# Performance work log

Measured on AMD Instinct MI355X. Metric: run time of the kernel, lower is better.

## Reference

```python
import jax, jax.numpy as jnp
import numpy as np

E = 32      # num_embodiments
A = 64      # action_dim
H = 1024    # hidden_size
B = 64
T = 64


def setup_inputs() -> dict:
    key = jax.random.key(0)
    ks = jax.random.split(key, 9)
    return {
        "actions": jax.random.normal(ks[0], (B, T, A), dtype=jnp.float32),
        "W1_W": 0.02 * jax.random.normal(ks[1], (E, A, H), dtype=jnp.float32),
        "W1_b": jnp.zeros((E, H), dtype=jnp.float32),
        "W2_W": 0.02 * jax.random.normal(ks[2], (E, 2 * H, H), dtype=jnp.float32),
        "W2_b": jnp.zeros((E, H), dtype=jnp.float32),
        "W3_W": 0.02 * jax.random.normal(ks[3], (E, H, H), dtype=jnp.float32),
        "W3_b": jnp.zeros((E, H), dtype=jnp.float32),
        "timesteps": jax.random.randint(ks[4], (B,), 0, 1000, dtype=jnp.int32),
        "cat_ids": jax.random.randint(ks[5], (B,), 0, E, dtype=jnp.int32),
    }


def _cat_linear(x, W, b, cat_ids):
    # x: (B,T,in), W: (E,in,out), b: (E,out)
    Wg = W[cat_ids]               # (B,in,out) gathered per-batch weights
    bg = b[cat_ids]               # (B,out)
    return jnp.einsum('bti,bio->bto', x, Wg) + bg[:, None, :]


def _sinusoidal_pe(t, dim):
    # t: (B,T) float -> (B,T,dim)
    half = dim // 2
    exponent = -jnp.arange(half, dtype=jnp.float32) * (jnp.log(jnp.float32(10000.0)) / half)
    freqs = t[..., None] * jnp.exp(exponent)
    return jnp.concatenate([jnp.sin(freqs), jnp.cos(freqs)], axis=-1)


def reference(actions, W1_W, W1_b, W2_W, W2_b, W3_W, W3_b, timesteps, cat_ids):
    b, t, _ = actions.shape
    ts = jnp.broadcast_to(timesteps.astype(jnp.float32)[:, None], (b, t))  # (B,T)
    a_emb = _cat_linear(actions, W1_W, W1_b, cat_ids)                      # (B,T,H)
    tau_emb = _sinusoidal_pe(ts, H).astype(a_emb.dtype)                    # (B,T,H)
    x = jnp.concatenate([a_emb, tau_emb], axis=-1)                         # (B,T,2H)
    h = _cat_linear(x, W2_W, W2_b, cat_ids)
    x = h * jax.nn.sigmoid(h)                                              # swish
    return _cat_linear(x, W3_W, W3_b, cat_ids)                             # (B,T,H)
```

## Files before the change

kernel.cpp:

```cpp
#include <hip/hip_runtime.h>
#include <hip/hip_bf16.h>

#define NB 64
#define NT 64
#define NA 64
#define NH 1024
#define NE 32
#define K2DIM 2048

typedef unsigned short bf16_t;
typedef __attribute__((ext_vector_type(8))) short bf16x8;
typedef __attribute__((ext_vector_type(4))) short s16x4;
typedef __attribute__((ext_vector_type(4))) float f32x4;

__device__ __forceinline__ bf16_t f32_to_bf16(float f) {
    unsigned int u = __float_as_uint(f);
    u = (u + 0x7FFFu + ((u >> 16) & 1u)) >> 16;
    return (bf16_t)u;
}
__device__ __forceinline__ unsigned cvt2(float x, float y) {
    unsigned short a = __builtin_bit_cast(unsigned short, __float2bfloat16(x));
    unsigned short b = __builtin_bit_cast(unsigned short, __float2bfloat16(y));
    return (unsigned)a | ((unsigned)b << 16);
}

__global__ void make_groups(const int* __restrict__ cat_ids,
                            int* __restrict__ groups)
{
    __shared__ int keys[NB], order[NB], catv[NB];
    __shared__ int gcat[NB], gnb[NB], gb[NB][2];
    __shared__ int sng;

    const int tid = threadIdx.x;
    int c = cat_ids[tid];
    catv[tid] = c;
    keys[tid] = c * 64 + tid;
    __syncthreads();

    int mykey = keys[tid];
    int rank = 0;
    for (int j = 0; j < NB; ++j) rank += (keys[j] < mykey) ? 1 : 0;
    order[rank] = tid;
    __syncthreads();

    if (tid == 0) {
        int ng = 0, prev = -1, cnt = 2;
        for (int i = 0; i < NB; ++i) {
            int b  = order[i];
            int cb = catv[b];
            if (cb != prev || cnt == 2) {
                gcat[ng] = cb; gnb[ng] = 0; cnt = 0; prev = cb; ++ng;
            }
            gb[ng - 1][cnt] = b;
            ++cnt; gnb[ng - 1] = cnt;
        }
        sng = ng;
    }
    __syncthreads();

    int ng = sng;
    int base = tid * 8;
    if (tid < ng) {
        int nbv = gnb[tid];
        groups[base + 0] = gcat[tid];
        groups[base + 1] = nbv;
        groups[base + 2] = gb[tid][0];
        groups[base + 3] = (nbv > 1) ? gb[tid][1] : gb[tid][0];
        groups[base + 4] = 0; groups[base + 5] = 0;
        groups[base + 6] = 0; groups[base + 7] = 0;
    } else {
        #pragma unroll
        for (int s = 0; s < 8; ++s) groups[base + s] = 0;
    }
}

__global__ __launch_bounds__(256) void k1_embed(
    const float* __restrict__ actions, const float* __restrict__ W1,
    const float* __restrict__ b1, const int* __restrict__ timesteps,
    const int* __restrict__ cat_ids, bf16_t* __restrict__ x)
{
    __shared__ float act[NT][NA];
    __shared__ float pe[64];

    const int b   = blockIdx.x;
    const int c0  = blockIdx.y * 64;
    const int tid = threadIdx.x;
    const int cat = cat_ids[b];
    const float ts = (float)timesteps[b];

    const float* ab = actions + b * (NT * NA);
    #pragma unroll
    for (int p = 0; p < 16; ++p) {
        int idx = tid + p * 256;
        act[idx >> 6][idx & 63] = ab[idx];
    }
    if (tid < 64) {
        const float kfreq = logf(10000.0f) / 512.0f;
        int c = c0 + tid;
        float v;
        if (c < 512) v = sinf(ts * expf(-(float)c * kfreq));
        else         v = cosf(ts * expf(-(float)(c - 512) * kfreq));
        pe[tid] = v;
    }
    __syncthreads();

    const int cc = tid & 63;
    const int c  = c0 + cc;
    const int t0 = tid >> 6;

    float acc[16];
    const float bias = b1[cat * NH + c];
    #pragma unroll
    for (int i = 0; i < 16; ++i) acc[i] = bias;

    const float* Wp = W1 + (size_t)cat * (NA * NH) + c;
    #pragma unroll 8
    for (int k = 0; k < NA; ++k) {
        float w = Wp[(size_t)k * NH];
        #pragma unroll
        for (int i = 0; i < 16; ++i)
            acc[i] = fmaf(act[t0 + 4 * i][k], w, acc[i]);
    }

    bf16_t* xb = x + (size_t)b * (NT * K2DIM);
    const bf16_t pv = f32_to_bf16(pe[cc]);
    #pragma unroll
    for (int i = 0; i < 16; ++i) {
        int t = t0 + 4 * i;
        xb[(size_t)t * K2DIM + c]      = f32_to_bf16(acc[i]);
        xb[(size_t)t * K2DIM + NH + c] = pv;
    }
}

template<int KDIM, bool SWISH, typename OutT>
__global__ __launch_bounds__(512, 4) void gemm_g2(
    const bf16_t* __restrict__ xin, const float* __restrict__ W,
    const float* __restrict__ bias, const int* __restrict__ groups,
    OutT* __restrict__ out)
{
    __shared__ __align__(128) char lds[2][12288];

    const int* grp = groups + blockIdx.y * 8;
    const int nb = grp[1];
    if (nb == 0) return;
    const int cat = grp[0];
    const int ba = grp[2];
    const int bb = grp[3];

    const int n0   = blockIdx.x * 64;
    const int tid  = threadIdx.x;
    const int lane = tid & 63;
    const int wv   = tid >> 6;
    const int l15  = lane & 15;
    const int l4   = lane >> 4;
    const int slot = wv >> 2;
    const int nf   = wv & 3;

    constexpr int NCH = KDIM / 32;

    const int xs_s = tid >> 8;
    const int xid  = tid & 255;
    const int xt   = xid >> 2;
    const int xoct = xid & 3;
    const bf16_t* xg = xin + ((size_t)(xs_s ? bb : ba) * NT + xt) * KDIM + xoct * 8;
    const int xl = xs_s * 4096 + xoct * 1024 + xt * 16;

    const int wk  = tid >> 4;
    const int wq4 = tid & 15;
    const float* wg = W + (size_t)cat * KDIM * NH + (size_t)wk * NH + n0 + wq4 * 4;
    const int wl = 8192 + ((wk >> 2) * 4 + (wq4 >> 2)) * 128
                        + (wk & 3) * 32 + (wq4 & 3) * 8;

    f32x4 acc[4];
    {
        float bv = bias[(size_t)cat * NH + n0 + nf * 16 + l15];
        #pragma unroll
        for (int mf = 0; mf < 4; ++mf) acc[mf] = (f32x4){bv, bv, bv, bv};
    }

    const unsigned ldsbase = (unsigned)(unsigned long long)&lds[0][0];
    const unsigned trb = ldsbase + 8192u + (unsigned)(l4 * 1024 + nf * 128 + l15 * 8);
    const int aoff = slot * 4096 + l4 * 1024 + l15 * 16;

    uint4  xr;
    float4 wr;
    auto LOAD = [&](int kc) {
        xr = *(const uint4*)(xg + (size_t)kc * 32);
        wr = *(const float4*)(wg + (size_t)kc * 32 * NH);
    };
    auto WRITE = [&](int pw) {
        *(uint4*)(&lds[pw][0] + xl) = xr;
        uint2 pk;
        pk.x = cvt2(wr.x, wr.y);
        pk.y = cvt2(wr.z, wr.w);
        *(uint2*)(&lds[pw][0] + wl) = pk;
    };

    LOAD(0);
    WRITE(0);
    LOAD(1);

    for (int kc = 0; kc < NCH; ++kc) {
        const int p = kc & 1;
        __syncthreads();

        bf16x8 af0 = *(const bf16x8*)(&lds[p][0] + aoff);
        bf16x8 af1 = *(const bf16x8*)(&lds[p][0] + aoff + 256);
        bf16x8 af2 = *(const bf16x8*)(&lds[p][0] + aoff + 512);
        bf16x8 af3 = *(const bf16x8*)(&lds[p][0] + aoff + 768);
        unsigned a = trb + (unsigned)(p * 12288);
        s16x4 lo, hi;
        asm volatile("ds_read_b64_tr_b16 %0, %1" : "=v"(lo) : "v"(a));
        asm volatile("ds_read_b64_tr_b16 %0, %1 offset:512" : "=v"(hi) : "v"(a));
        bf16x8 bfr = __builtin_shufflevector(lo, hi, 0, 1, 2, 3, 4, 5, 6, 7);

        asm volatile("s_waitcnt lgkmcnt(0)" ::: "memory");
        __builtin_amdgcn_sched_barrier(0);
        acc[0] = __builtin_amdgcn_mfma_f32_16x16x32_bf16(af0, bfr, acc[0], 0, 0, 0);
        acc[1] = __builtin_amdgcn_mfma_f32_16x16x32_bf16(af1, bfr, acc[1], 0, 0, 0);
        acc[2] = __builtin_amdgcn_mfma_f32_16x16x32_bf16(af2, bfr, acc[2], 0, 0, 0);
        acc[3] = __builtin_amdgcn_mfma_f32_16x16x32_bf16(af3, bfr, acc[3], 0, 0, 0);

        if (kc + 1 < NCH) WRITE(p ^ 1);
        if (kc + 2 < NCH) LOAD(kc + 2);
    }

    if (slot < nb) {
        const int bout = slot ? bb : ba;
        const int col  = n0 + nf * 16 + l15;
        #pragma unroll
        for (int mf = 0; mf < 4; ++mf) {
            #pragma unroll
            for (int r = 0; r < 4; ++r) {
                int trow = mf * 16 + l4 * 4 + r;
                float h = acc[mf][r];
                if (SWISH) h = h / (1.0f + __expf(-h));
                if constexpr (sizeof(OutT) == 2) {
                    out[((size_t)bout * NT + trow) * NH + col] = (OutT)f32_to_bf16(h);
                } else {
                    out[((size_t)bout * NT + trow) * NH + col] = h;
                }
            }
        }
    }
}

extern "C" void kernel_launch(void* const* d_in, const int* in_sizes, int n_in,
                              void* d_out, int out_size, void* d_ws, size_t ws_size,
                              hipStream_t stream) {
    const float* actions   = (const float*)d_in[0];
    const float* W1        = (const float*)d_in[1];
    const float* b1        = (const float*)d_in[2];
    const float* W2        = (const float*)d_in[3];
    const float* b2        = (const float*)d_in[4];
    const float* W3        = (const float*)d_in[5];
    const float* b3        = (const float*)d_in[6];
    const int*   timesteps = (const int*)d_in[7];
    const int*   cat_ids   = (const int*)d_in[8];
    float* out = (float*)d_out;

    bf16_t* x = (bf16_t*)d_ws;
    bf16_t* y = x + (size_t)NB * NT * K2DIM;
    int* groups = (int*)(y + (size_t)NB * NT * NH);

    make_groups<<<1, 64, 0, stream>>>(cat_ids, groups);
    k1_embed<<<dim3(NB, NH / 64), 256, 0, stream>>>(actions, W1, b1, timesteps, cat_ids, x);
    gemm_g2<K2DIM, true,  bf16_t><<<dim3(16, 64), 512, 0, stream>>>(x, W2, b2, groups, y);
    gemm_g2<NH,    false, float ><<<dim3(16, 64), 512, 0, stream>>>(y, W3, b3, groups, out);
}
```

Baseline: 176.7 us.

## Narrow grouped GEMM N tile to 32, double K chunk, deepen weight prefetch

The grouped GEMM kernels now use 256-thread blocks that each cover 32 output columns instead of 64, which doubles the grid to 32x64 blocks. Each K step now processes 64 instead of 32, with two MFMA substeps per LDS buffer. Weights are prefetched two chunks ahead in registers, with the loop manually unrolled over ping-pong buffers. The aim is more blocks in flight and better latency hiding for the fp32 weight stream, at the cost of more LDS per block, more registers, and activation tiles being reloaded by twice as many blocks.

```diff
diff --git a/kernel.cpp b/kernel.cpp
--- a/kernel.cpp
+++ b/kernel.cpp
@@ -133,12 +133,12 @@
 }
 
 template<int KDIM, bool SWISH, typename OutT>
-__global__ __launch_bounds__(512, 4) void gemm_g2(
+__global__ __launch_bounds__(256, 3) void gemm_g2p(
     const bf16_t* __restrict__ xin, const float* __restrict__ W,
     const float* __restrict__ bias, const int* __restrict__ groups,
     OutT* __restrict__ out)
 {
-    __shared__ __align__(128) char lds[2][12288];
+    __shared__ __align__(128) char lds[2][20480];
 
     const int* grp = groups + blockIdx.y * 8;
     const int nb = grp[1];
@@ -147,29 +147,28 @@
     const int ba = grp[2];
     const int bb = grp[3];
 
-    const int n0   = blockIdx.x * 64;
+    const int n0   = blockIdx.x * 32;
     const int tid  = threadIdx.x;
     const int lane = tid & 63;
     const int wv   = tid >> 6;
     const int l15  = lane & 15;
     const int l4   = lane >> 4;
-    const int slot = wv >> 2;
-    const int nf   = wv & 3;
-
-    constexpr int NCH = KDIM / 32;
-
-    const int xs_s = tid >> 8;
-    const int xid  = tid & 255;
-    const int xt   = xid >> 2;
-    const int xoct = xid & 3;
-    const bf16_t* xg = xin + ((size_t)(xs_s ? bb : ba) * NT + xt) * KDIM + xoct * 8;
-    const int xl = xs_s * 4096 + xoct * 1024 + xt * 16;
-
-    const int wk  = tid >> 4;
-    const int wq4 = tid & 15;
-    const float* wg = W + (size_t)cat * KDIM * NH + (size_t)wk * NH + n0 + wq4 * 4;
-    const int wl = 8192 + ((wk >> 2) * 4 + (wq4 >> 2)) * 128
-                        + (wk & 3) * 32 + (wq4 & 3) * 8;
+    const int slot = wv >> 1;
+    const int nf   = wv & 1;
+
+    constexpr int NCH = KDIM / 64;
+
+    const int xs_s = tid >> 7;
+    const int xt   = (tid >> 1) & 63;
+    const int xoh  = tid & 1;
+    const bf16_t* xg = xin + ((size_t)(xs_s ? bb : ba) * NT + xt) * KDIM + xoh * 32;
+    const int xl = xs_s * 8192 + xoh * 4096 + xt * 16;
+
+    const int wk   = tid >> 2;
+    const int woct = tid & 3;
+    const float* wg = W + (size_t)cat * KDIM * NH + (size_t)wk * NH + n0 + woct * 8;
+    const int wl = 16384 + (wk >> 5) * 2048 + ((wk & 31) >> 2) * 256
+                 + (woct >> 1) * 128 + (wk & 3) * 32 + (woct & 1) * 16;
 
     f32x4 acc[4];
     {
@@ -179,50 +178,77 @@
     }
 
     const unsigned ldsbase = (unsigned)(unsigned long long)&lds[0][0];
-    const unsigned trb = ldsbase + 8192u + (unsigned)(l4 * 1024 + nf * 128 + l15 * 8);
-    const int aoff = slot * 4096 + l4 * 1024 + l15 * 16;
-
-    uint4  xr;
-    float4 wr;
-    auto LOAD = [&](int kc) {
-        xr = *(const uint4*)(xg + (size_t)kc * 32);
-        wr = *(const float4*)(wg + (size_t)kc * 32 * NH);
-    };
-    auto WRITE = [&](int pw) {
-        *(uint4*)(&lds[pw][0] + xl) = xr;
-        uint2 pk;
-        pk.x = cvt2(wr.x, wr.y);
-        pk.y = cvt2(wr.z, wr.w);
-        *(uint2*)(&lds[pw][0] + wl) = pk;
-    };
-
-    LOAD(0);
-    WRITE(0);
-    LOAD(1);
-
-    for (int kc = 0; kc < NCH; ++kc) {
-        const int p = kc & 1;
+    const unsigned trb0 = ldsbase + 16384u
+                        + (unsigned)(l4 * 512 + nf * 128 + l15 * 8);
+    const int aoff = slot * 8192 + l4 * 1024 + l15 * 16;
+
+    uint4  xr[4];
+    float4 wa[2], wb[2];
+
+    auto XLOAD = [&](int c) {
+        int i = c < NCH ? c : NCH - 1;
+        const bf16_t* s = xg + (size_t)i * 64;
+        #pragma unroll
+        for (int p_ = 0; p_ < 4; ++p_) xr[p_] = *(const uint4*)(s + p_ * 8);
+    };
+    auto XWRITE = [&](char* buf) {
+        #pragma unroll
+        for (int p_ = 0; p_ < 4; ++p_)
+            *(uint4*)(buf + xl + p_ * 1024) = xr[p_];
+    };
+    auto WLOAD = [&](float4* w, int c) {
+        int i = c < NCH ? c : NCH - 1;
+        const float* s = wg + (size_t)i * 64 * NH;
+        w[0] = *(const float4*)(s);
+        w[1] = *(const float4*)(s + 4);
+    };
+    auto WWRITE = [&](char* buf, const float4* w) {
+        uint4 pk;
+        pk.x = cvt2(w[0].x, w[0].y);
+        pk.y = cvt2(w[0].z, w[0].w);
+        pk.z = cvt2(w[1].x, w[1].y);
+        pk.w = cvt2(w[1].z, w[1].w);
+        *(uint4*)(buf + wl) = pk;
+    };
+    auto COMPUTE = [&](int p) {
+        char* buf = &lds[0][0] + p * 20480;
+        unsigned trp = trb0 + (unsigned)(p * 20480);
+        #pragma unroll
+        for (int ks = 0; ks < 2; ++ks) {
+            bf16x8 af[4];
+            #pragma unroll
+            for (int mf = 0; mf < 4; ++mf)
+                af[mf] = *(const bf16x8*)(buf + aoff + ks * 4096 + mf * 256);
+            unsigned a = trp + (unsigned)(ks * 2048);
+            s16x4 lo, hi;
+            asm volatile("ds_read_b64_tr_b16 %0, %1" : "=v"(lo) : "v"(a));
+            asm volatile("ds_read_b64_tr_b16 %0, %1 offset:256" : "=v"(hi) : "v"(a));
+            bf16x8 bfr = __builtin_shufflevector(lo, hi, 0, 1, 2, 3, 4, 5, 6, 7);
+            asm volatile("s_waitcnt lgkmcnt(0)" ::: "memory");
+            __builtin_amdgcn_sched_barrier(0);
+            #pragma unroll
+            for (int mf = 0; mf < 4; ++mf)
+                acc[mf] = __builtin_amdgcn_mfma_f32_16x16x32_bf16(
+                    af[mf], bfr, acc[mf], 0, 0, 0);
+        }
+    };
+
+    char* buf0 = &lds[0][0];
+    char* buf1 = &lds[0][0] + 20480;
+
+    WLOAD(wa, 0); WLOAD(wb, 1); XLOAD(0);
+    WWRITE(buf0, wa); XWRITE(buf0);
+    WLOAD(wa, 2); XLOAD(1);
+
+    for (int kc = 0; kc < NCH; kc += 2) {
         __syncthreads();
-
-        bf16x8 af0 = *(const bf16x8*)(&lds[p][0] + aoff);
-        bf16x8 af1 = *(const bf16x8*)(&lds[p][0] + aoff + 256);
-        bf16x8 af2 = *(const bf16x8*)(&lds[p][0] + aoff + 512);
-        bf16x8 af3 = *(const bf16x8*)(&lds[p][0] + aoff + 768);
-        unsigned a = trb + (unsigned)(p * 12288);
-        s16x4 lo, hi;
-        asm volatile("ds_read_b64_tr_b16 %0, %1" : "=v"(lo) : "v"(a));
-        asm volatile("ds_read_b64_tr_b16 %0, %1 offset:512" : "=v"(hi) : "v"(a));
-        bf16x8 bfr = __builtin_shufflevector(lo, hi, 0, 1, 2, 3, 4, 5, 6, 7);
-
-        asm volatile("s_waitcnt lgkmcnt(0)" ::: "memory");
-        __builtin_amdgcn_sched_barrier(0);
-        acc[0] = __builtin_amdgcn_mfma_f32_16x16x32_bf16(af0, bfr, acc[0], 0, 0, 0);
-        acc[1] = __builtin_amdgcn_mfma_f32_16x16x32_bf16(af1, bfr, acc[1], 0, 0, 0);
-        acc[2] = __builtin_amdgcn_mfma_f32_16x16x32_bf16(af2, bfr, acc[2], 0, 0, 0);
-        acc[3] = __builtin_amdgcn_mfma_f32_16x16x32_bf16(af3, bfr, acc[3], 0, 0, 0);
-
-        if (kc + 1 < NCH) WRITE(p ^ 1);
-        if (kc + 2 < NCH) LOAD(kc + 2);
+        COMPUTE(0);
+        WWRITE(buf1, wb); XWRITE(buf1);
+        WLOAD(wb, kc + 3); XLOAD(kc + 2);
+        __syncthreads();
+        COMPUTE(1);
+        WWRITE(buf0, wa); XWRITE(buf0);
+        WLOAD(wa, kc + 4); XLOAD(kc + 3);
     }
 
     if (slot < nb) {
@@ -265,6 +291,6 @@
 
     make_groups<<<1, 64, 0, stream>>>(cat_ids, groups);
     k1_embed<<<dim3(NB, NH / 64), 256, 0, stream>>>(actions, W1, b1, timesteps, cat_ids, x);
-    gemm_g2<K2DIM, true,  bf16_t><<<dim3(16, 64), 512, 0, stream>>>(x, W2, b2, groups, y);
-    gemm_g2<NH,    false, float ><<<dim3(16, 64), 512, 0, stream>>>(y, W3, b3, groups, out);
-}
+    gemm_g2p<K2DIM, true,  bf16_t><<<dim3(32, 64), 256, 0, stream>>>(x, W2, b2, groups, y);
+    gemm_g2p<NH,    false, float ><<<dim3(32, 64), 256, 0, stream>>>(y, W3, b3, groups, out);
+}
```

New measurement: 395.3 us. 2.24x slower.

## Group up to four batches per category and stream weights via LDS per wave

Applied to the files above, without the earlier changes.

Batches are now grouped up to four per embodiment instead of two, so each block reuses one weight tile across more batches and fewer redundant weight reads hit global memory. The GEMM is restructured: each of four waves owns one batch and computes a full 64x64 output tile. Activations are loaded straight from global memory into registers, and only the weights are staged in LDS, in 64-wide K chunks with a double-buffered register prefetch. The risks are higher register pressure from 16 accumulators and uncoalesced direct activation loads.

```diff
diff --git a/kernel.cpp b/kernel.cpp
--- a/kernel.cpp
+++ b/kernel.cpp
@@ -28,7 +28,7 @@
                             int* __restrict__ groups)
 {
     __shared__ int keys[NB], order[NB], catv[NB];
-    __shared__ int gcat[NB], gnb[NB], gb[NB][2];
+    __shared__ int gcat[NB], gnb[NB], gb[NB][4];
     __shared__ int sng;
 
     const int tid = threadIdx.x;
@@ -44,11 +44,11 @@
     __syncthreads();
 
     if (tid == 0) {
-        int ng = 0, prev = -1, cnt = 2;
+        int ng = 0, prev = -1, cnt = 4;
         for (int i = 0; i < NB; ++i) {
             int b  = order[i];
             int cb = catv[b];
-            if (cb != prev || cnt == 2) {
+            if (cb != prev || cnt == 4) {
                 gcat[ng] = cb; gnb[ng] = 0; cnt = 0; prev = cb; ++ng;
             }
             gb[ng - 1][cnt] = b;
@@ -64,9 +64,9 @@
         int nbv = gnb[tid];
         groups[base + 0] = gcat[tid];
         groups[base + 1] = nbv;
-        groups[base + 2] = gb[tid][0];
-        groups[base + 3] = (nbv > 1) ? gb[tid][1] : gb[tid][0];
-        groups[base + 4] = 0; groups[base + 5] = 0;
+        #pragma unroll
+        for (int s = 0; s < 4; ++s)
+            groups[base + 2 + s] = gb[tid][s < nbv ? s : 0];
         groups[base + 6] = 0; groups[base + 7] = 0;
     } else {
         #pragma unroll
@@ -133,19 +133,17 @@
 }
 
 template<int KDIM, bool SWISH, typename OutT>
-__global__ __launch_bounds__(512, 4) void gemm_g2(
+__global__ __launch_bounds__(256) void gemm_wstream(
     const bf16_t* __restrict__ xin, const float* __restrict__ W,
     const float* __restrict__ bias, const int* __restrict__ groups,
     OutT* __restrict__ out)
 {
-    __shared__ __align__(128) char lds[2][12288];
+    __shared__ __align__(128) char wlds[2][8192];
 
     const int* grp = groups + blockIdx.y * 8;
-    const int nb = grp[1];
-    if (nb == 0) return;
+    const int mult = grp[1];
+    if (mult == 0) return;
     const int cat = grp[0];
-    const int ba = grp[2];
-    const int bb = grp[3];
 
     const int n0   = blockIdx.x * 64;
     const int tid  = threadIdx.x;
@@ -153,92 +151,145 @@
     const int wv   = tid >> 6;
     const int l15  = lane & 15;
     const int l4   = lane >> 4;
-    const int slot = wv >> 2;
-    const int nf   = wv & 3;
-
-    constexpr int NCH = KDIM / 32;
-
-    const int xs_s = tid >> 8;
-    const int xid  = tid & 255;
-    const int xt   = xid >> 2;
-    const int xoct = xid & 3;
-    const bf16_t* xg = xin + ((size_t)(xs_s ? bb : ba) * NT + xt) * KDIM + xoct * 8;
-    const int xl = xs_s * 4096 + xoct * 1024 + xt * 16;
-
-    const int wk  = tid >> 4;
-    const int wq4 = tid & 15;
-    const float* wg = W + (size_t)cat * KDIM * NH + (size_t)wk * NH + n0 + wq4 * 4;
-    const int wl = 8192 + ((wk >> 2) * 4 + (wq4 >> 2)) * 128
-                        + (wk & 3) * 32 + (wq4 & 3) * 8;
-
-    f32x4 acc[4];
-    {
+    const int myb  = grp[2 + wv];
+
+    constexpr int NCH = KDIM / 64;
+
+    const int wo8 = tid & 7;
+    const int wk0 = tid >> 3;
+    const float* wg = W + (size_t)cat * KDIM * NH + (size_t)wk0 * NH + n0 + wo8 * 8;
+    const int wl0 = ((wk0 >> 2) * 512) + ((wo8 >> 1) * 128)
+                  + ((wk0 & 3) * 32) + ((wo8 & 1) * 16);
+
+    const bf16_t* xa = xin + ((size_t)myb * NT + l15) * KDIM + l4 * 8;
+
+    f32x4 acc[4][4];
+    #pragma unroll
+    for (int nf = 0; nf < 4; ++nf) {
         float bv = bias[(size_t)cat * NH + n0 + nf * 16 + l15];
         #pragma unroll
-        for (int mf = 0; mf < 4; ++mf) acc[mf] = (f32x4){bv, bv, bv, bv};
-    }
-
-    const unsigned ldsbase = (unsigned)(unsigned long long)&lds[0][0];
-    const unsigned trb = ldsbase + 8192u + (unsigned)(l4 * 1024 + nf * 128 + l15 * 8);
-    const int aoff = slot * 4096 + l4 * 1024 + l15 * 16;
-
-    uint4  xr;
-    float4 wr;
-    auto LOAD = [&](int kc) {
-        xr = *(const uint4*)(xg + (size_t)kc * 32);
-        wr = *(const float4*)(wg + (size_t)kc * 32 * NH);
-    };
-    auto WRITE = [&](int pw) {
-        *(uint4*)(&lds[pw][0] + xl) = xr;
-        uint2 pk;
-        pk.x = cvt2(wr.x, wr.y);
-        pk.y = cvt2(wr.z, wr.w);
-        *(uint2*)(&lds[pw][0] + wl) = pk;
-    };
-
-    LOAD(0);
-    WRITE(0);
-    LOAD(1);
-
-    for (int kc = 0; kc < NCH; ++kc) {
-        const int p = kc & 1;
-        __syncthreads();
-
-        bf16x8 af0 = *(const bf16x8*)(&lds[p][0] + aoff);
-        bf16x8 af1 = *(const bf16x8*)(&lds[p][0] + aoff + 256);
-        bf16x8 af2 = *(const bf16x8*)(&lds[p][0] + aoff + 512);
-        bf16x8 af3 = *(const bf16x8*)(&lds[p][0] + aoff + 768);
-        unsigned a = trb + (unsigned)(p * 12288);
-        s16x4 lo, hi;
-        asm volatile("ds_read_b64_tr_b16 %0, %1" : "=v"(lo) : "v"(a));
-        asm volatile("ds_read_b64_tr_b16 %0, %1 offset:512" : "=v"(hi) : "v"(a));
-        bf16x8 bfr = __builtin_shufflevector(lo, hi, 0, 1, 2, 3, 4, 5, 6, 7);
-
+        for (int m = 0; m < 4; ++m) acc[m][nf] = (f32x4){bv, bv, bv, bv};
+    }
+
+    const unsigned lbase = (unsigned)(unsigned long long)&wlds[0][0];
+    const unsigned trb   = lbase + (unsigned)(l4 * 1024 + l15 * 8);
+
+    float4 qa0, qa1, qa2, qa3, qb0, qb1, qb2, qb3;
+    bf16x8 a0s0, a1s0, a2s0, a3s0, a0s1, a1s1, a2s1, a3s1;
+
+#define WLQ(r0, r1, r2, r3, c) do { int i_ = (c) < NCH ? (c) : NCH - 1;       \
+        const float* s_ = wg + (size_t)i_ * 64 * NH;                          \
+        r0 = *(const float4*)(s_);                                            \
+        r1 = *(const float4*)(s_ + 4);                                        \
+        r2 = *(const float4*)(s_ + (size_t)32 * NH);                          \
+        r3 = *(const float4*)(s_ + (size_t)32 * NH + 4); } while (0)
+#define WSQ(p, r0, r1, r2, r3) do { char* bp_ = &wlds[p][0];                  \
+        uint4 u_;                                                             \
+        u_.x = cvt2(r0.x, r0.y); u_.y = cvt2(r0.z, r0.w);                     \
+        u_.z = cvt2(r1.x, r1.y); u_.w = cvt2(r1.z, r1.w);                     \
+        *(uint4*)(bp_ + wl0) = u_;                                            \
+        u_.x = cvt2(r2.x, r2.y); u_.y = cvt2(r2.z, r2.w);                     \
+        u_.z = cvt2(r3.x, r3.y); u_.w = cvt2(r3.z, r3.w);                     \
+        *(uint4*)(bp_ + wl0 + 4096) = u_; } while (0)
+#define ALD(c) do { const bf16_t* s_ = xa + (size_t)(c) * 64;                 \
+        a0s0 = *(const bf16x8*)(s_);                                          \
+        a1s0 = *(const bf16x8*)(s_ + (size_t)16 * KDIM);                      \
+        a2s0 = *(const bf16x8*)(s_ + (size_t)32 * KDIM);                      \
+        a3s0 = *(const bf16x8*)(s_ + (size_t)48 * KDIM);                      \
+        a0s1 = *(const bf16x8*)(s_ + 32);                                     \
+        a1s1 = *(const bf16x8*)(s_ + (size_t)16 * KDIM + 32);                 \
+        a2s1 = *(const bf16x8*)(s_ + (size_t)32 * KDIM + 32);                 \
+        a3s1 = *(const bf16x8*)(s_ + (size_t)48 * KDIM + 32); } while (0)
+#define MF(d, A, B) d = __builtin_amdgcn_mfma_f32_16x16x32_bf16(A, B, d, 0, 0, 0)
+#define TRPAIR(lo_, hi_, addr_, off_) do {                                    \
+        asm volatile("ds_read_b64_tr_b16 %0, %1 offset:" #off_               \
+                     : "=v"(lo_) : "v"(addr_));                               \
+        asm volatile("ds_read_b64_tr_b16 %0, %1 offset:" #off_ "+512"        \
+                     : "=v"(hi_) : "v"(addr_)); } while (0)
+#define CMP(p) do {                                                           \
+        unsigned ab_ = trb + (p) * 8192u;                                     \
+        s16x4 lo0, hi0, lo1, hi1, lo2, hi2, lo3, hi3;                         \
+        TRPAIR(lo0, hi0, ab_, 0);                                             \
+        TRPAIR(lo1, hi1, ab_, 128);                                           \
+        TRPAIR(lo2, hi2, ab_, 256);                                           \
+        TRPAIR(lo3, hi3, ab_, 384);                                           \
+        asm volatile("s_waitcnt lgkmcnt(0)" ::: "memory");                    \
+        __builtin_amdgcn_sched_barrier(0);                                    \
+        {   bf16x8 b0 = __builtin_shufflevector(lo0, hi0, 0,1,2,3,4,5,6,7);   \
+            bf16x8 b1 = __builtin_shufflevector(lo1, hi1, 0,1,2,3,4,5,6,7);   \
+            bf16x8 b2 = __builtin_shufflevector(lo2, hi2, 0,1,2,3,4,5,6,7);   \
+            bf16x8 b3 = __builtin_shufflevector(lo3, hi3, 0,1,2,3,4,5,6,7);   \
+            MF(acc[0][0], a0s0, b0); MF(acc[1][0], a1s0, b0);                 \
+            MF(acc[2][0], a2s0, b0); MF(acc[3][0], a3s0, b0);                 \
+            MF(acc[0][1], a0s0, b1); MF(acc[1][1], a1s0, b1);                 \
+            MF(acc[2][1], a2s0, b1); MF(acc[3][1], a3s0, b1);                 \
+            MF(acc[0][2], a0s0, b2); MF(acc[1][2], a1s0, b2);                 \
+            MF(acc[2][2], a2s0, b2); MF(acc[3][2], a3s0, b2);                 \
+            MF(acc[0][3], a0s0, b3); MF(acc[1][3], a1s0, b3);                 \
+            MF(acc[2][3], a2s0, b3); MF(acc[3][3], a3s0, b3); }               \
+        unsigned ab2_ = ab_ + 4096u;                                          \
+        TRPAIR(lo0, hi0, ab2_, 0);                                            \
+        TRPAIR(lo1, hi1, ab2_, 128);                                          \
+        TRPAIR(lo2, hi2, ab2_, 256);                                          \
+        TRPAIR(lo3, hi3, ab2_, 384);                                          \
+        asm volatile("s_waitcnt lgkmcnt(0)" ::: "memory");                    \
+        __builtin_amdgcn_sched_barrier(0);                                    \
+        {   bf16x8 b0 = __builtin_shufflevector(lo0, hi0, 0,1,2,3,4,5,6,7);   \
+            bf16x8 b1 = __builtin_shufflevector(lo1, hi1, 0,1,2,3,4,5,6,7);   \
+            bf16x8 b2 = __builtin_shufflevector(lo2, hi2, 0,1,2,3,4,5,6,7);   \
+            bf16x8 b3 = __builtin_shufflevector(lo3, hi3, 0,1,2,3,4,5,6,7);   \
+            MF(acc[0][0], a0s1, b0); MF(acc[1][0], a1s1, b0);                 \
+            MF(acc[2][0], a2s1, b0); MF(acc[3][0], a3s1, b0);                 \
+            MF(acc[0][1], a0s1, b1); MF(acc[1][1], a1s1, b1);                 \
+            MF(acc[2][1], a2s1, b1); MF(acc[3][1], a3s1, b1);                 \
+            MF(acc[0][2], a0s1, b2); MF(acc[1][2], a1s1, b2);                 \
+            MF(acc[2][2], a2s1, b2); MF(acc[3][2], a3s1, b2);                 \
+            MF(acc[0][3], a0s1, b3); MF(acc[1][3], a1s1, b3);                 \
+            MF(acc[2][3], a2s1, b3); MF(acc[3][3], a3s1, b3); }               \
+    } while (0)
+
+    WLQ(qa0, qa1, qa2, qa3, 0);
+    WLQ(qb0, qb1, qb2, qb3, 1);
+
+    for (int kc = 0; kc < NCH; kc += 2) {
+        WSQ(0, qa0, qa1, qa2, qa3);
+        ALD(kc);
+        __builtin_amdgcn_sched_barrier(0);
+        WLQ(qa0, qa1, qa2, qa3, kc + 2);
         asm volatile("s_waitcnt lgkmcnt(0)" ::: "memory");
+        __builtin_amdgcn_s_barrier();
+        CMP(0);
+        WSQ(1, qb0, qb1, qb2, qb3);
+        ALD(kc + 1);
         __builtin_amdgcn_sched_barrier(0);
-        acc[0] = __builtin_amdgcn_mfma_f32_16x16x32_bf16(af0, bfr, acc[0], 0, 0, 0);
-        acc[1] = __builtin_amdgcn_mfma_f32_16x16x32_bf16(af1, bfr, acc[1], 0, 0, 0);
-        acc[2] = __builtin_amdgcn_mfma_f32_16x16x32_bf16(af2, bfr, acc[2], 0, 0, 0);
-        acc[3] = __builtin_amdgcn_mfma_f32_16x16x32_bf16(af3, bfr, acc[3], 0, 0, 0);
-
-        if (kc + 1 < NCH) WRITE(p ^ 1);
-        if (kc + 2 < NCH) LOAD(kc + 2);
-    }
-
-    if (slot < nb) {
-        const int bout = slot ? bb : ba;
-        const int col  = n0 + nf * 16 + l15;
-        #pragma unroll
-        for (int mf = 0; mf < 4; ++mf) {
+        WLQ(qb0, qb1, qb2, qb3, kc + 3);
+        asm volatile("s_waitcnt lgkmcnt(0)" ::: "memory");
+        __builtin_amdgcn_s_barrier();
+        CMP(1);
+    }
+#undef WLQ
+#undef WSQ
+#undef ALD
+#undef MF
+#undef TRPAIR
+#undef CMP
+
+    if (wv < mult) {
+        #pragma unroll
+        for (int m = 0; m < 4; ++m) {
             #pragma unroll
-            for (int r = 0; r < 4; ++r) {
-                int trow = mf * 16 + l4 * 4 + r;
-                float h = acc[mf][r];
-                if (SWISH) h = h / (1.0f + __expf(-h));
-                if constexpr (sizeof(OutT) == 2) {
-                    out[((size_t)bout * NT + trow) * NH + col] = (OutT)f32_to_bf16(h);
-                } else {
-                    out[((size_t)bout * NT + trow) * NH + col] = h;
+            for (int nf = 0; nf < 4; ++nf) {
+                int col = n0 + nf * 16 + l15;
+                #pragma unroll
+                for (int r = 0; r < 4; ++r) {
+                    int row = m * 16 + l4 * 4 + r;
+                    float h = acc[m][nf][r];
+                    if (SWISH) h = h / (1.0f + __expf(-h));
+                    if constexpr (sizeof(OutT) == 2) {
+                        out[((size_t)myb * NT + row) * NH + col] = (OutT)f32_to_bf16(h);
+                    } else {
+                        out[((size_t)myb * NT + row) * NH + col] = h;
+                    }
                 }
             }
         }
@@ -265,6 +316,6 @@
 
     make_groups<<<1, 64, 0, stream>>>(cat_ids, groups);
     k1_embed<<<dim3(NB, NH / 64), 256, 0, stream>>>(actions, W1, b1, timesteps, cat_ids, x);
-    gemm_g2<K2DIM, true,  bf16_t><<<dim3(16, 64), 512, 0, stream>>>(x, W2, b2, groups, y);
-    gemm_g2<NH,    false, float ><<<dim3(16, 64), 512, 0, stream>>>(y, W3, b3, groups, out);
-}
+    gemm_wstream<K2DIM, true,  bf16_t><<<dim3(16, 64), 256, 0, stream>>>(x, W2, b2, groups, y);
+    gemm_wstream<NH,    false, float ><<<dim3(16, 64), 256, 0, stream>>>(y, W3, b3, groups, out);
+}
```

New measurement: 176.5 us. Within noise of the previous version (-0.2%).
